# Performance work log

Measured on AMD Instinct MI355X. Metric: run time of the kernel, lower is better.

Reference implementation:

```python
import jax, jax.numpy as jnp
import numpy as np

N = 30000      # nodes
E = 480000     # edges (avg degree 16)
IN = 128       # atom in_channels
ED = 16        # edge_dim
D = 128        # hidden_channels
OUT = 64       # out_channels
L = 4          # num_layers + 1 GCNEConv layers


def setup_inputs() -> dict:
    key = jax.random.key(0)
    ks = jax.random.split(key, 8)
    w = lambda k, sh: (jax.random.normal(k, sh, dtype=jnp.float32) * 0.05)
    return {
        "x": jax.random.normal(ks[0], (N, IN), dtype=jnp.float32),
        "edge_index": jax.random.randint(ks[1], (2, E), 0, N, dtype=jnp.int64),
        "edge_attr": jax.random.normal(ks[2], (E, ED), dtype=jnp.float32),
        "W_atom": w(ks[3], (IN, D)), "b_atom": jnp.zeros((D,), jnp.float32),
        "W_bond": w(ks[4], (ED, D)), "b_bond": jnp.zeros((D,), jnp.float32),
        "W_seq": w(ks[5], (L, D, D)), "b_seq": jnp.zeros((L, D), jnp.float32),
        "W_lin": w(ks[6], (2 * D, OUT)), "b_lin": jnp.zeros((OUT,), jnp.float32),
    }


def _aggregate(h_bond, idx_i, n):
    # CMPNN 'message_booster': elementwise sum_agg * max_agg over incoming edges
    sum_agg = jax.ops.segment_sum(h_bond, idx_i, num_segments=n)
    max_agg = jax.ops.segment_max(h_bond, idx_i, num_segments=n)
    max_agg = jnp.where(jnp.isfinite(max_agg), max_agg, 0.0)  # empty segments -> 0
    return sum_agg * max_agg


def reference(x, edge_index, edge_attr, W_atom, b_atom, W_bond, b_bond,
              W_seq, b_seq, W_lin, b_lin):
    n = x.shape[0]
    idx_i = edge_index[0]  # flow='target_to_source' -> i is edge_index[0]
    idx_j = edge_index[1]

    x_proj = jax.nn.relu(x @ W_atom + b_atom)          # [N, D]
    h_atom = x_proj
    h_bond = jax.nn.relu(edge_attr @ W_bond + b_bond)  # [E, D]

    # first L-1 convs: node update + edge update
    for l in range(L - 1):
        msg = _aggregate(h_bond, idx_i, n)             # [N, D]
        h_atom = h_atom * msg                          # inner_product communicator
        # edge_update: x[edge_index_i] - edge_attr[edge_index_j] (node-index gather
        # into edge tensor, faithful to the original code; valid since E > N)
        bond = h_atom[idx_i] - h_bond[idx_j]           # [E, D]
        h_bond = jax.nn.relu(bond @ W_seq[l] + b_seq[l])

    # last conv: only the node output is used downstream
    msg = _aggregate(h_bond, idx_i, n)
    aggr_atom_message = h_atom * msg

    # top-level communicator (inner_product): hidden_state * message
    h_atom = h_atom * aggr_atom_message
    out = jnp.concatenate([h_atom, x_proj], axis=1) @ W_lin + b_lin  # [N, OUT]
    return out
```

## Files before the change

### kernel.cpp

```cpp
#include <hip/hip_runtime.h>
#include <hip/hip_bf16.h>

#define DD 128
#define SCB 256
#define CE  512
#define CB  512

typedef __attribute__((ext_vector_type(8))) short bf16x8;
typedef __attribute__((ext_vector_type(4))) float f32x4;

__device__ __forceinline__ unsigned bf16_rne(float f) {
    unsigned u = __float_as_uint(f);
    return (u + 0x7fffu + ((u >> 16) & 1u)) >> 16;
}

__global__ __launch_bounds__(256)
void hist_kernel(const int* __restrict__ idx_i, int* __restrict__ cnt, int E)
{
    const int e = blockIdx.x * 256 + threadIdx.x;
    if (e < E) atomicAdd(&cnt[idx_i[e]], 1);
}

__global__ __launch_bounds__(SCB)
void scan1_kernel(const int* __restrict__ cnt, int* __restrict__ exc,
                  int* __restrict__ bsum, int n)
{
    __shared__ int s[SCB];
    const int i = blockIdx.x * SCB + (int)threadIdx.x;
    const int v = (i < n) ? cnt[i] : 0;
    s[threadIdx.x] = v;
    __syncthreads();
    #pragma unroll
    for (int off = 1; off < SCB; off <<= 1) {
        int t = (threadIdx.x >= off) ? s[threadIdx.x - off] : 0;
        __syncthreads();
        s[threadIdx.x] += t;
        __syncthreads();
    }
    if (i < n) exc[i] = s[threadIdx.x] - v;
    if (threadIdx.x == SCB - 1) bsum[blockIdx.x] = s[threadIdx.x];
}

__global__ __launch_bounds__(SCB)
void scan2_kernel(int* __restrict__ bsum, int nb)
{
    __shared__ int s[SCB];
    const int v = (threadIdx.x < nb) ? bsum[threadIdx.x] : 0;
    s[threadIdx.x] = v;
    __syncthreads();
    #pragma unroll
    for (int off = 1; off < SCB; off <<= 1) {
        int t = (threadIdx.x >= off) ? s[threadIdx.x - off] : 0;
        __syncthreads();
        s[threadIdx.x] += t;
        __syncthreads();
    }
    if (threadIdx.x < nb) bsum[threadIdx.x] = s[threadIdx.x] - v;
}

__global__ __launch_bounds__(SCB)
void scan3_kernel(int* __restrict__ exc, const int* __restrict__ bsum, int n)
{
    const int i = blockIdx.x * SCB + (int)threadIdx.x;
    if (i < n) exc[i] += bsum[i >> 8];
}

__global__ __launch_bounds__(256)
void scatter_kernel(const int* __restrict__ idx_i, const int* __restrict__ idx_j,
                    int* __restrict__ cursor, int* __restrict__ perm,
                    int* __restrict__ si, int* __restrict__ sj, int E)
{
    const int e = blockIdx.x * 256 + threadIdx.x;
    if (e < E) {
        const int n = idx_i[e];
        const int p = atomicAdd(&cursor[n], 1);
        perm[p] = e;
        si[p] = n;
        sj[p] = idx_j[e];
    }
}

__global__ __launch_bounds__(1024)
void gemm128_mfma_kernel(float* __restrict__ A0, const float* __restrict__ A1,
                         int nA, int nTotal,
                         const float* __restrict__ W, const float* __restrict__ bias,
                         int bias_limit, int do_relu, int update,
                         float* __restrict__ sum_agg, int* __restrict__ max_agg,
                         float* __restrict__ out0, float* __restrict__ out1,
                         int ntiles)
{
    __shared__ __align__(16) unsigned char SM[131584];
    char*  const Whi = (char*)SM;
    char*  const Wlo = (char*)SM + 32768;
    char*  const Ahi = (char*)SM + 65536;
    char*  const Alo = (char*)SM + 98304;
    float* const Wf  = (float*)(SM + 65536);
    float* const bs  = (float*)(SM + 131072);

    const int t = (int)threadIdx.x;

    {
        const float4* Wg = (const float4*)W;
        float4* Wd = (float4*)Wf;
        #pragma unroll
        for (int i = 0; i < 4; ++i) Wd[t + i * 1024] = Wg[t + i * 1024];
        if (t < DD) bs[t] = bias ? bias[t] : 0.f;
    }
    __syncthreads();
    {
        const int col = t >> 3;
        const int kb  = (t & 7) * 16;
        unsigned h16[16], l16[16];
        #pragma unroll
        for (int j = 0; j < 16; ++j) {
            const float w = Wf[(size_t)(kb + j) * DD + col];
            const unsigned hb = bf16_rne(w);
            const float hf = __uint_as_float(hb << 16);
            h16[j] = hb;
            l16[j] = bf16_rne(w - hf);
        }
        #pragma unroll
        for (int c = 0; c < 2; ++c) {
            uint4 ph, pl;
            ph.x = h16[c*8+0] | (h16[c*8+1] << 16);
            ph.y = h16[c*8+2] | (h16[c*8+3] << 16);
            ph.z = h16[c*8+4] | (h16[c*8+5] << 16);
            ph.w = h16[c*8+6] | (h16[c*8+7] << 16);
            pl.x = l16[c*8+0] | (l16[c*8+1] << 16);
            pl.y = l16[c*8+2] | (l16[c*8+3] << 16);
            pl.z = l16[c*8+4] | (l16[c*8+5] << 16);
            pl.w = l16[c*8+6] | (l16[c*8+7] << 16);
            const int off = ((col * 256 + (kb + c * 8) * 2)) ^ ((col & 7) << 4);
            *(uint4*)(Whi + off) = ph;
            *(uint4*)(Wlo + off) = pl;
        }
    }

    const int w  = t >> 6;
    const int l  = t & 63;
    const int wm = w >> 2;
    const int wn = w & 3;
    const int g  = l >> 4;
    const int q  = l & 15;

    for (int tile = blockIdx.x; tile < ntiles; tile += gridDim.x) {
        const int e0 = tile * 128;
        __syncthreads();

        #pragma unroll
        for (int i = 0; i < 2; ++i) {
            const int task = t + i * 1024;
            const int row  = task >> 4;
            const int c    = task & 15;
            const int rr = min(e0 + row, nTotal - 1);
            float d[8];
            if (rr < nA) {
                float* ph0 = A0 + (size_t)rr * DD + c * 8;
                const float4 a0 = *(const float4*)ph0;
                const float4 a1 = *(const float4*)(ph0 + 4);
                if (update) {
                    float* sp = sum_agg + (size_t)rr * DD + c * 8;
                    int*   mp = max_agg + (size_t)rr * DD + c * 8;
                    const float4 s0 = *(const float4*)sp;
                    const float4 s1 = *(const float4*)(sp + 4);
                    const int4   m0 = *(const int4*)mp;
                    const int4   m1 = *(const int4*)(mp + 4);
                    d[0] = a0.x * s0.x * __int_as_float(m0.x);
                    d[1] = a0.y * s0.y * __int_as_float(m0.y);
                    d[2] = a0.z * s0.z * __int_as_float(m0.z);
                    d[3] = a0.w * s0.w * __int_as_float(m0.w);
                    d[4] = a1.x * s1.x * __int_as_float(m1.x);
                    d[5] = a1.y * s1.y * __int_as_float(m1.y);
                    d[6] = a1.z * s1.z * __int_as_float(m1.z);
                    d[7] = a1.w * s1.w * __int_as_float(m1.w);
                    *(float4*)ph0       = make_float4(d[0], d[1], d[2], d[3]);
                    *(float4*)(ph0 + 4) = make_float4(d[4], d[5], d[6], d[7]);
                    *(float4*)sp       = make_float4(0.f, 0.f, 0.f, 0.f);
                    *(float4*)(sp + 4) = make_float4(0.f, 0.f, 0.f, 0.f);
                    *(int4*)mp       = make_int4(0, 0, 0, 0);
                    *(int4*)(mp + 4) = make_int4(0, 0, 0, 0);
                } else {
                    d[0] = a0.x; d[1] = a0.y; d[2] = a0.z; d[3] = a0.w;
                    d[4] = a1.x; d[5] = a1.y; d[6] = a1.z; d[7] = a1.w;
                }
            } else {
                const float* pa = A1 + (size_t)(rr - nA) * DD + c * 8;
                const float4 a0 = *(const float4*)pa;
                const float4 a1 = *(const float4*)(pa + 4);
                d[0] = a0.x; d[1] = a0.y; d[2] = a0.z; d[3] = a0.w;
                d[4] = a1.x; d[5] = a1.y; d[6] = a1.z; d[7] = a1.w;
            }
            unsigned h8[8], l8[8];
            #pragma unroll
            for (int j = 0; j < 8; ++j) {
                const unsigned hb = bf16_rne(d[j]);
                const float hf = __uint_as_float(hb << 16);
                h8[j] = hb;
                l8[j] = bf16_rne(d[j] - hf);
            }
            uint4 ph, pl;
            ph.x = h8[0] | (h8[1] << 16);
            ph.y = h8[2] | (h8[3] << 16);
            ph.z = h8[4] | (h8[5] << 16);
            ph.w = h8[6] | (h8[7] << 16);
            pl.x = l8[0] | (l8[1] << 16);
            pl.y = l8[2] | (l8[3] << 16);
            pl.z = l8[4] | (l8[5] << 16);
            pl.w = l8[6] | (l8[7] << 16);
            const int off = ((row * 256 + c * 16)) ^ ((row & 7) << 4);
            *(uint4*)(Ahi + off) = ph;
            *(uint4*)(Alo + off) = pl;
        }
        __syncthreads();

        f32x4 acc[2][2];
        const f32x4 zero = {0.f, 0.f, 0.f, 0.f};
        acc[0][0] = zero; acc[0][1] = zero; acc[1][0] = zero; acc[1][1] = zero;

        #pragma unroll
        for (int ks = 0; ks < 4; ++ks) {
            const int kbyte = ks * 64 + g * 16;
            bf16x8 ah[2], al[2], bh[2], bl[2];
            #pragma unroll
            for (int m = 0; m < 2; ++m) {
                const int row = wm * 32 + m * 16 + q;
                const int off = (row * 256 + kbyte) ^ ((row & 7) << 4);
                ah[m] = *(const bf16x8*)(Ahi + off);
                al[m] = *(const bf16x8*)(Alo + off);
            }
            #pragma unroll
            for (int n = 0; n < 2; ++n) {
                const int colv = wn * 32 + n * 16 + q;
                const int off = (colv * 256 + kbyte) ^ ((colv & 7) << 4);
                bh[n] = *(const bf16x8*)(Whi + off);
                bl[n] = *(const bf16x8*)(Wlo + off);
            }
            #pragma unroll
            for (int m = 0; m < 2; ++m)
                #pragma unroll
                for (int n = 0; n < 2; ++n)
                    acc[m][n] = __builtin_amdgcn_mfma_f32_16x16x32_bf16(ah[m], bh[n], acc[m][n], 0, 0, 0);
            #pragma unroll
            for (int m = 0; m < 2; ++m)
                #pragma unroll
                for (int n = 0; n < 2; ++n)
                    acc[m][n] = __builtin_amdgcn_mfma_f32_16x16x32_bf16(ah[m], bl[n], acc[m][n], 0, 0, 0);
            #pragma unroll
            for (int m = 0; m < 2; ++m)
                #pragma unroll
                for (int n = 0; n < 2; ++n)
                    acc[m][n] = __builtin_amdgcn_mfma_f32_16x16x32_bf16(al[m], bh[n], acc[m][n], 0, 0, 0);
        }

        #pragma unroll
        for (int n = 0; n < 2; ++n) {
            const int colv = wn * 32 + n * 16 + q;
            const float bv = bs[colv];
            #pragma unroll
            for (int m = 0; m < 2; ++m) {
                #pragma unroll
                for (int r = 0; r < 4; ++r) {
                    const int row = e0 + wm * 32 + m * 16 + g * 4 + r;
                    if (row < nTotal) {
                        float v = acc[m][n][r] + ((row < bias_limit) ? bv : 0.f);
                        if (do_relu) v = fmaxf(v, 0.f);
                        out0[(size_t)row * DD + colv] = v;
                        if (out1) out1[(size_t)row * DD + colv] = v;
                    }
                }
            }
        }
    }
}

__global__ __launch_bounds__(512)
void bond_pass_kernel(const float* __restrict__ edge_attr,
                      const float* __restrict__ Wb, const float* __restrict__ bb,
                      const int* __restrict__ si, const int* __restrict__ perm,
                      float* __restrict__ h_head0,
                      float* __restrict__ sum_agg, int* __restrict__ max_agg,
                      int E, int N)
{
    __shared__ __align__(16) float ea_s[CB][16];
    __shared__ int si_s[CB], pm_s[CB];

    const int p0b = blockIdx.x * CB;
    if (p0b >= E) return;
    const int t = (int)threadIdx.x;

    for (int i = t; i < CB; i += 512) {
        const int p = min(p0b + i, E - 1);
        si_s[i] = si[p];
        pm_s[i] = perm[p];
    }
    for (int task = t; task < CB * 4; task += 512) {
        const int row = task >> 2;
        const int c4  = task & 3;
        const int p = min(p0b + row, E - 1);
        const int orig = perm[p];
        *(float4*)(&ea_s[row][c4 * 4]) =
            *(const float4*)(edge_attr + (size_t)orig * 16 + c4 * 4);
    }
    __syncthreads();

    const int w    = t >> 6;
    const int lane = t & 63;
    const int c    = lane * 2;
    const int q0   = w * 64;
    const int pg0  = p0b + q0;
    if (pg0 >= E) return;

    float wc0[16], wc1[16];
    #pragma unroll
    for (int k = 0; k < 16; ++k) {
        const float2 wv = *(const float2*)(Wb + k * DD + c);
        wc0[k] = wv.x; wc1[k] = wv.y;
    }
    const float2 bc = *(const float2*)(bb + c);

    const int firstNode = si_s[q0];
    const int lastNode  = si_s[q0 + 63];

    int curNode = firstNode;
    float2 rs = make_float2(0.f, 0.f), rm = make_float2(0.f, 0.f);

    #define BP_FLUSH()                                                           \
    {                                                                            \
        if (curNode == firstNode || curNode == lastNode) {                       \
            atomicAdd(&sum_agg[(size_t)curNode * DD + c],     rs.x);             \
            atomicAdd(&sum_agg[(size_t)curNode * DD + c + 1], rs.y);             \
            atomicMax(&max_agg[(size_t)curNode * DD + c],     __float_as_int(rm.x)); \
            atomicMax(&max_agg[(size_t)curNode * DD + c + 1], __float_as_int(rm.y)); \
        } else {                                                                 \
            *(float2*)(sum_agg + (size_t)curNode * DD + c) = rs;                 \
            *(int2*)(max_agg + (size_t)curNode * DD + c) =                       \
                make_int2(__float_as_int(rm.x), __float_as_int(rm.y));           \
        }                                                                        \
    }

    #pragma unroll 4
    for (int kk = 0; kk < 64; ++kk) {
        const int i = si_s[q0 + kk];
        if (i != curNode) {
            BP_FLUSH();
            curNode = i;
            rs = make_float2(0.f, 0.f);
            rm = make_float2(0.f, 0.f);
        }
        const float4* ear = (const float4*)(&ea_s[q0 + kk][0]);
        const float4 e0 = ear[0], e1 = ear[1], e2 = ear[2], e3 = ear[3];
        float ax = bc.x, ay = bc.y;
        ax = fmaf(e0.x, wc0[ 0], ax);  ay = fmaf(e0.x, wc1[ 0], ay);
        ax = fmaf(e0.y, wc0[ 1], ax);  ay = fmaf(e0.y, wc1[ 1], ay);
        ax = fmaf(e0.z, wc0[ 2], ax);  ay = fmaf(e0.z, wc1[ 2], ay);
        ax = fmaf(e0.w, wc0[ 3], ax);  ay = fmaf(e0.w, wc1[ 3], ay);
        ax = fmaf(e1.x, wc0[ 4], ax);  ay = fmaf(e1.x, wc1[ 4], ay);
        ax = fmaf(e1.y, wc0[ 5], ax);  ay = fmaf(e1.y, wc1[ 5], ay);
        ax = fmaf(e1.z, wc0[ 6], ax);  ay = fmaf(e1.z, wc1[ 6], ay);
        ax = fmaf(e1.w, wc0[ 7], ax);  ay = fmaf(e1.w, wc1[ 7], ay);
        ax = fmaf(e2.x, wc0[ 8], ax);  ay = fmaf(e2.x, wc1[ 8], ay);
        ax = fmaf(e2.y, wc0[ 9], ax);  ay = fmaf(e2.y, wc1[ 9], ay);
        ax = fmaf(e2.z, wc0[10], ax);  ay = fmaf(e2.z, wc1[10], ay);
        ax = fmaf(e2.w, wc0[11], ax);  ay = fmaf(e2.w, wc1[11], ay);
        ax = fmaf(e3.x, wc0[12], ax);  ay = fmaf(e3.x, wc1[12], ay);
        ax = fmaf(e3.y, wc0[13], ax);  ay = fmaf(e3.y, wc1[13], ay);
        ax = fmaf(e3.z, wc0[14], ax);  ay = fmaf(e3.z, wc1[14], ay);
        ax = fmaf(e3.w, wc0[15], ax);  ay = fmaf(e3.w, wc1[15], ay);
        float2 v;
        v.x = fmaxf(ax, 0.f);
        v.y = fmaxf(ay, 0.f);
        if (pg0 + kk >= E) { v.x = 0.f; v.y = 0.f; }
        rs.x += v.x; rs.y += v.y;
        rm.x = fmaxf(rm.x, v.x); rm.y = fmaxf(rm.y, v.y);
        if (pg0 + kk < E) {
            const int orig = pm_s[q0 + kk];
            if (orig < N) *(float2*)(h_head0 + (size_t)orig * DD + c) = v;
        }
    }
    BP_FLUSH();
    #undef BP_FLUSH
}

__global__ __launch_bounds__(512)
void edge_pass_kernel(const float* __restrict__ PQ,
                      const int* __restrict__ si, const int* __restrict__ sj,
                      const int* __restrict__ perm,
                      float* __restrict__ head_next, int store_head,
                      float* __restrict__ sum_agg, int* __restrict__ max_agg,
                      int E, int N)
{
    __shared__ int si_s[CE], sj_s[CE], pm_s[CE];
    const int p0b = blockIdx.x * CE;
    if (p0b >= E) return;
    const int t = (int)threadIdx.x;
    for (int i = t; i < CE; i += 512) {
        const int p = min(p0b + i, E - 1);
        si_s[i] = si[p];
        sj_s[i] = sj[p];
        pm_s[i] = perm[p];
    }
    __syncthreads();

    const int w    = t >> 6;
    const int lane = t & 63;
    const int c    = lane * 2;
    const int q0   = w * 64;
    const int pg0  = p0b + q0;
    if (pg0 >= E) return;

    const int firstNode = si_s[q0];
    const int lastNode  = si_s[q0 + 63];

    const float* __restrict__ Qbase = PQ + (size_t)N * DD + c;

    float2 qa = *(const float2*)(Qbase + (size_t)sj_s[q0 + 0] * DD);
    float2 qb = *(const float2*)(Qbase + (size_t)sj_s[q0 + 1] * DD);
    float2 qc = *(const float2*)(Qbase + (size_t)sj_s[q0 + 2] * DD);
    float2 qd = *(const float2*)(Qbase + (size_t)sj_s[q0 + 3] * DD);
    float2 qe = *(const float2*)(Qbase + (size_t)sj_s[q0 + 4] * DD);
    float2 qf = *(const float2*)(Qbase + (size_t)sj_s[q0 + 5] * DD);
    float2 qg = *(const float2*)(Qbase + (size_t)sj_s[q0 + 6] * DD);
    float2 qh = *(const float2*)(Qbase + (size_t)sj_s[q0 + 7] * DD);

    int curNode = firstNode;
    float2 Pi = *(const float2*)(PQ + (size_t)curNode * DD + c);
    float2 rs = make_float2(0.f, 0.f), rm = make_float2(0.f, 0.f);

    #define EP_FLUSH()                                                           \
    {                                                                            \
        if (curNode == firstNode || curNode == lastNode) {                       \
            atomicAdd(&sum_agg[(size_t)curNode * DD + c],     rs.x);             \
            atomicAdd(&sum_agg[(size_t)curNode * DD + c + 1], rs.y);             \
            atomicMax(&max_agg[(size_t)curNode * DD + c],     __float_as_int(rm.x)); \
            atomicMax(&max_agg[(size_t)curNode * DD + c + 1], __float_as_int(rm.y)); \
        } else {                                                                 \
            *(float2*)(sum_agg + (size_t)curNode * DD + c) = rs;                 \
            *(int2*)(max_agg + (size_t)curNode * DD + c) =                       \
                make_int2(__float_as_int(rm.x), __float_as_int(rm.y));           \
        }                                                                        \
    }

    #define EP_STEP(K, QREG)                                                     \
    {                                                                            \
        const int kk = (K);                                                      \
        const int i = si_s[q0 + kk];                                             \
        if (i != curNode) {                                                      \
            EP_FLUSH();                                                          \
            curNode = i;                                                         \
            Pi = *(const float2*)(PQ + (size_t)i * DD + c);                      \
            rs = make_float2(0.f, 0.f);                                          \
            rm = make_float2(0.f, 0.f);                                          \
        }                                                                        \
        float2 v;                                                                \
        v.x = fmaxf(Pi.x - QREG.x, 0.f);                                         \
        v.y = fmaxf(Pi.y - QREG.y, 0.f);                                         \
        if (pg0 + kk >= E) { v.x = 0.f; v.y = 0.f; }                             \
        rs.x += v.x; rs.y += v.y;                                                \
        rm.x = fmaxf(rm.x, v.x); rm.y = fmaxf(rm.y, v.y);                        \
        if (store_head && (pg0 + kk) < E) {                                      \
            const int orig = pm_s[q0 + kk];                                      \
            if (orig < N) *(float2*)(head_next + (size_t)orig * DD + c) = v;     \
        }                                                                        \
        if (kk + 8 < 64)                                                         \
            QREG = *(const float2*)(Qbase + (size_t)sj_s[q0 + kk + 8] * DD);     \
    }

    #pragma unroll
    for (int k = 0; k < 64; k += 8) {
        EP_STEP(k + 0, qa);
        EP_STEP(k + 1, qb);
        EP_STEP(k + 2, qc);
        EP_STEP(k + 3, qd);
        EP_STEP(k + 4, qe);
        EP_STEP(k + 5, qf);
        EP_STEP(k + 6, qg);
        EP_STEP(k + 7, qh);
    }
    EP_FLUSH();
    #undef EP_STEP
    #undef EP_FLUSH
}

__global__ __launch_bounds__(512, 2)
void final_mfma_kernel(const float* __restrict__ h, const float* __restrict__ sum_agg,
                       const int* __restrict__ max_agg, const float* __restrict__ xp,
                       const float* __restrict__ Wl, const float* __restrict__ bl,
                       float* __restrict__ out, int N)
{
    __shared__ __align__(16) unsigned char SM[65808];
    char*  const Whi = (char*)SM;
    char*  const Wlo = (char*)SM + 32768;
    float* const Wf  = (float*)SM;
    float* const bs  = (float*)(SM + 65536);

    const int t = (int)threadIdx.x;
    {
        const float4* Wg = (const float4*)Wl;
        float4* Wd = (float4*)Wf;
        #pragma unroll
        for (int i = 0; i < 8; ++i) Wd[t + i * 512] = Wg[t + i * 512];
        if (t < 64) bs[t] = bl[t];
    }
    __syncthreads();
    {
        const int col = t & 63;
        const int kb  = (t >> 6) * 32;
        float v[32];
        #pragma unroll
        for (int j = 0; j < 32; ++j) v[j] = Wf[(size_t)(kb + j) * 64 + col];
        __syncthreads();
        #pragma unroll
        for (int c = 0; c < 4; ++c) {
            unsigned h8[8], l8[8];
            #pragma unroll
            for (int j = 0; j < 8; ++j) {
                const float w0 = v[c * 8 + j];
                const unsigned hb = bf16_rne(w0);
                h8[j] = hb;
                l8[j] = bf16_rne(w0 - __uint_as_float(hb << 16));
            }
            uint4 ph, pl;
            ph.x = h8[0] | (h8[1] << 16); ph.y = h8[2] | (h8[3] << 16);
            ph.z = h8[4] | (h8[5] << 16); ph.w = h8[6] | (h8[7] << 16);
            pl.x = l8[0] | (l8[1] << 16); pl.y = l8[2] | (l8[3] << 16);
            pl.z = l8[4] | (l8[5] << 16); pl.w = l8[6] | (l8[7] << 16);
            const int off = (col * 512 + (kb + c * 8) * 2) ^ ((col & 7) << 4);
            *(uint4*)(Whi + off) = ph;
            *(uint4*)(Wlo + off) = pl;
        }
    }
    __syncthreads();

    const int w  = t >> 6;
    const int l  = t & 63;
    const int wm = w >> 1;
    const int wn = w & 1;
    const int g  = l >> 4;
    const int q  = l & 15;
    const int r0 = (int)blockIdx.x * 128;

    f32x4 acc[2][2];
    const f32x4 zero = {0.f, 0.f, 0.f, 0.f};
    acc[0][0] = zero; acc[0][1] = zero; acc[1][0] = zero; acc[1][1] = zero;

    #pragma unroll
    for (int ks = 0; ks < 8; ++ks) {
        const int kf = (ks & 3) * 32 + g * 8;
        bf16x8 ah[2], al[2];
        #pragma unroll
        for (int m = 0; m < 2; ++m) {
            const int rr = min(r0 + wm * 32 + m * 16 + q, N - 1);
            float d[8];
            if (ks < 4) {
                const float* ph = h       + (size_t)rr * DD + kf;
                const float* ps = sum_agg + (size_t)rr * DD + kf;
                const int*   pm = max_agg + (size_t)rr * DD + kf;
                const float4 a0 = *(const float4*)ph;
                const float4 a1 = *(const float4*)(ph + 4);
                const float4 s0 = *(const float4*)ps;
                const float4 s1 = *(const float4*)(ps + 4);
                const int4   i0 = *(const int4*)pm;
                const int4   i1 = *(const int4*)(pm + 4);
                d[0] = a0.x * a0.x * s0.x * __int_as_float(i0.x);
                d[1] = a0.y * a0.y * s0.y * __int_as_float(i0.y);
                d[2] = a0.z * a0.z * s0.z * __int_as_float(i0.z);
                d[3] = a0.w * a0.w * s0.w * __int_as_float(i0.w);
                d[4] = a1.x * a1.x * s1.x * __int_as_float(i1.x);
                d[5] = a1.y * a1.y * s1.y * __int_as_float(i1.y);
                d[6] = a1.z * a1.z * s1.z * __int_as_float(i1.z);
                d[7] = a1.w * a1.w * s1.w * __int_as_float(i1.w);
            } else {
                const float* pa = xp + (size_t)rr * DD + kf;
                const float4 a0 = *(const float4*)pa;
                const float4 a1 = *(const float4*)(pa + 4);
                d[0] = a0.x; d[1] = a0.y; d[2] = a0.z; d[3] = a0.w;
                d[4] = a1.x; d[5] = a1.y; d[6] = a1.z; d[7] = a1.w;
            }
            unsigned h8[8], l8[8];
            #pragma unroll
            for (int j = 0; j < 8; ++j) {
                const unsigned hb = bf16_rne(d[j]);
                h8[j] = hb;
                l8[j] = bf16_rne(d[j] - __uint_as_float(hb << 16));
            }
            uint4 ph2, pl2;
            ph2.x = h8[0] | (h8[1] << 16); ph2.y = h8[2] | (h8[3] << 16);
            ph2.z = h8[4] | (h8[5] << 16); ph2.w = h8[6] | (h8[7] << 16);
            pl2.x = l8[0] | (l8[1] << 16); pl2.y = l8[2] | (l8[3] << 16);
            pl2.z = l8[4] | (l8[5] << 16); pl2.w = l8[6] | (l8[7] << 16);
            ah[m] = *(bf16x8*)&ph2;
            al[m] = *(bf16x8*)&pl2;
        }
        bf16x8 bh[2], blo[2];
        #pragma unroll
        for (int n = 0; n < 2; ++n) {
            const int colv = wn * 32 + n * 16 + q;
            const int off = (colv * 512 + ks * 64 + g * 16) ^ ((colv & 7) << 4);
            bh[n]  = *(const bf16x8*)(Whi + off);
            blo[n] = *(const bf16x8*)(Wlo + off);
        }
        #pragma unroll
        for (int m = 0; m < 2; ++m)
            #pragma unroll
            for (int n = 0; n < 2; ++n) {
                acc[m][n] = __builtin_amdgcn_mfma_f32_16x16x32_bf16(ah[m], bh[n],  acc[m][n], 0, 0, 0);
                acc[m][n] = __builtin_amdgcn_mfma_f32_16x16x32_bf16(ah[m], blo[n], acc[m][n], 0, 0, 0);
                acc[m][n] = __builtin_amdgcn_mfma_f32_16x16x32_bf16(al[m], bh[n],  acc[m][n], 0, 0, 0);
            }
    }

    #pragma unroll
    for (int n = 0; n < 2; ++n) {
        const int colv = wn * 32 + n * 16 + q;
        const float bv = bs[colv];
        #pragma unroll
        for (int m = 0; m < 2; ++m) {
            #pragma unroll
            for (int r = 0; r < 4; ++r) {
                const int row = r0 + wm * 32 + m * 16 + g * 4 + r;
                if (row < N) out[(size_t)row * 64 + colv] = acc[m][n][r] + bv;
            }
        }
    }
}

extern "C" void kernel_launch(void* const* d_in, const int* in_sizes, int n_in,
                              void* d_out, int out_size, void* d_ws, size_t ws_size,
                              hipStream_t stream)
{
    const float* x         = (const float*)d_in[0];
    const int*   edge_idx  = (const int*)d_in[1];
    const float* edge_attr = (const float*)d_in[2];
    const float* W_atom    = (const float*)d_in[3];
    const float* b_atom    = (const float*)d_in[4];
    const float* W_bond    = (const float*)d_in[5];
    const float* b_bond    = (const float*)d_in[6];
    const float* W_seq     = (const float*)d_in[7];
    const float* b_seq     = (const float*)d_in[8];
    const float* W_lin     = (const float*)d_in[9];
    const float* b_lin     = (const float*)d_in[10];
    float* out = (float*)d_out;

    const int N = in_sizes[0] / DD;
    const int E = in_sizes[1] / 2;
    const int* idx_i = edge_idx;
    const int* idx_j = edge_idx + E;

    const size_t nd = (size_t)N * DD;
    float* ws      = (float*)d_ws;
    float* x_proj  = ws;
    float* h_atom  = x_proj + nd;
    float* head    = h_atom + nd;
    float* sum_agg = head + nd;
    int*   max_agg = (int*)(sum_agg + nd);
    float* PQ      = (float*)(max_agg + nd);
    int*   cnt     = (int*)(PQ + 2 * nd);
    int*   cursor  = cnt + N;
    int*   bsum    = cursor + N;
    int*   perm    = bsum + 256;
    int*   si      = perm + E;
    int*   sj      = si + E;

    hipMemsetAsync(cnt, 0, (size_t)N * 4, stream);
    hist_kernel<<<(E + 255) / 256, 256, 0, stream>>>(idx_i, cnt, E);
    const int nb_scan = (N + SCB - 1) / SCB;
    scan1_kernel<<<nb_scan, SCB, 0, stream>>>(cnt, cursor, bsum, N);
    scan2_kernel<<<1, SCB, 0, stream>>>(bsum, nb_scan);
    scan3_kernel<<<nb_scan, SCB, 0, stream>>>(cursor, bsum, N);
    scatter_kernel<<<(E + 255) / 256, 256, 0, stream>>>(idx_i, idx_j, cursor, perm, si, sj, E);

    hipMemsetAsync(sum_agg, 0, nd * 4, stream);
    hipMemsetAsync(max_agg, 0, nd * 4, stream);

    const int ntiles_n = (N + 127) / 128;
    gemm128_mfma_kernel<<<min(ntiles_n, 256), 1024, 0, stream>>>(
        (float*)x, x, N, N, W_atom, b_atom, N, 1, 0, nullptr, nullptr,
        x_proj, h_atom, ntiles_n);

    bond_pass_kernel<<<(E + CB - 1) / CB, 512, 0, stream>>>(
        edge_attr, W_bond, b_bond, si, perm, head, sum_agg, max_agg, E, N);

    const int ntiles_pq = (2 * N + 127) / 128;
    const int ep_blocks = (E + CE - 1) / CE;
    for (int l = 0; l < 3; ++l) {
        gemm128_mfma_kernel<<<256, 1024, 0, stream>>>(
            h_atom, head, N, 2 * N, W_seq + (size_t)l * DD * DD,
            b_seq + (size_t)l * DD, N, 0, 1, sum_agg, max_agg,
            PQ, nullptr, ntiles_pq);
        edge_pass_kernel<<<ep_blocks, 512, 0, stream>>>(
            PQ, si, sj, perm, head, (l < 2) ? 1 : 0, sum_agg, max_agg, E, N);
    }

    final_mfma_kernel<<<(N + 127) / 128, 512, 0, stream>>>(
        h_atom, sum_agg, (const int*)max_agg, x_proj, W_lin, b_lin, out, N);
}
```

Measured before the change: 395.3 us.

## Keep split-bf16 weights in registers and shrink GEMM blocks to 512 threads

The 128x128 GEMM kernel no longer stages the fp32 weight matrix and its hi/lo bf16 split in LDS. Each wave now owns a 16-column slice and keeps its hi/lo weight fragments in registers, while shared memory holds only the A tile (64KB instead of about 128KB). Blocks drop to 512 threads with one tile each, launching a full grid instead of a persistent 256-block grid. This removes the shared-memory weight reads and raises possible occupancy. The cost is that every block re-reads and re-splits W from global memory, and each wave now holds 8 accumulators plus weight registers, which raises register pressure.

```diff
diff --git a/kernel.cpp b/kernel.cpp
--- a/kernel.cpp
+++ b/kernel.cpp
@@ -80,7 +80,7 @@
     }
 }
 
-__global__ __launch_bounds__(1024)
+__global__ __launch_bounds__(512, 4)
 void gemm128_mfma_kernel(float* __restrict__ A0, const float* __restrict__ A1,
                          int nA, int nTotal,
                          const float* __restrict__ W, const float* __restrict__ bias,
@@ -89,67 +89,45 @@
                          float* __restrict__ out0, float* __restrict__ out1,
                          int ntiles)
 {
-    __shared__ __align__(16) unsigned char SM[131584];
-    char*  const Whi = (char*)SM;
-    char*  const Wlo = (char*)SM + 32768;
-    char*  const Ahi = (char*)SM + 65536;
-    char*  const Alo = (char*)SM + 98304;
-    float* const Wf  = (float*)(SM + 65536);
-    float* const bs  = (float*)(SM + 131072);
+    __shared__ __align__(16) unsigned char SM[65536];
+    char* const Ahi = (char*)SM;
+    char* const Alo = (char*)SM + 32768;
 
     const int t = (int)threadIdx.x;
-
-    {
-        const float4* Wg = (const float4*)W;
-        float4* Wd = (float4*)Wf;
-        #pragma unroll
-        for (int i = 0; i < 4; ++i) Wd[t + i * 1024] = Wg[t + i * 1024];
-        if (t < DD) bs[t] = bias ? bias[t] : 0.f;
-    }
-    __syncthreads();
-    {
-        const int col = t >> 3;
-        const int kb  = (t & 7) * 16;
-        unsigned h16[16], l16[16];
-        #pragma unroll
-        for (int j = 0; j < 16; ++j) {
-            const float w = Wf[(size_t)(kb + j) * DD + col];
-            const unsigned hb = bf16_rne(w);
-            const float hf = __uint_as_float(hb << 16);
-            h16[j] = hb;
-            l16[j] = bf16_rne(w - hf);
-        }
-        #pragma unroll
-        for (int c = 0; c < 2; ++c) {
-            uint4 ph, pl;
-            ph.x = h16[c*8+0] | (h16[c*8+1] << 16);
-            ph.y = h16[c*8+2] | (h16[c*8+3] << 16);
-            ph.z = h16[c*8+4] | (h16[c*8+5] << 16);
-            ph.w = h16[c*8+6] | (h16[c*8+7] << 16);
-            pl.x = l16[c*8+0] | (l16[c*8+1] << 16);
-            pl.y = l16[c*8+2] | (l16[c*8+3] << 16);
-            pl.z = l16[c*8+4] | (l16[c*8+5] << 16);
-            pl.w = l16[c*8+6] | (l16[c*8+7] << 16);
-            const int off = ((col * 256 + (kb + c * 8) * 2)) ^ ((col & 7) << 4);
-            *(uint4*)(Whi + off) = ph;
-            *(uint4*)(Wlo + off) = pl;
-        }
-    }
-
-    const int w  = t >> 6;
-    const int l  = t & 63;
-    const int wm = w >> 2;
-    const int wn = w & 3;
-    const int g  = l >> 4;
-    const int q  = l & 15;
+    const int w = t >> 6;
+    const int l = t & 63;
+    const int g = l >> 4;
+    const int q = l & 15;
+    const int colv = w * 16 + q;
+
+    bf16x8 wh[4], wl[4];
+    #pragma unroll
+    for (int ks = 0; ks < 4; ++ks) {
+        unsigned h8[8], l8[8];
+        #pragma unroll
+        for (int j = 0; j < 8; ++j) {
+            const float w0 = W[(size_t)(ks * 32 + g * 8 + j) * DD + colv];
+            const unsigned hb = bf16_rne(w0);
+            h8[j] = hb;
+            l8[j] = bf16_rne(w0 - __uint_as_float(hb << 16));
+        }
+        uint4 ph, pl;
+        ph.x = h8[0] | (h8[1] << 16); ph.y = h8[2] | (h8[3] << 16);
+        ph.z = h8[4] | (h8[5] << 16); ph.w = h8[6] | (h8[7] << 16);
+        pl.x = l8[0] | (l8[1] << 16); pl.y = l8[2] | (l8[3] << 16);
+        pl.z = l8[4] | (l8[5] << 16); pl.w = l8[6] | (l8[7] << 16);
+        wh[ks] = *(bf16x8*)&ph;
+        wl[ks] = *(bf16x8*)&pl;
+    }
+    const float bv = bias ? bias[colv] : 0.f;
 
     for (int tile = blockIdx.x; tile < ntiles; tile += gridDim.x) {
         const int e0 = tile * 128;
         __syncthreads();
 
         #pragma unroll
-        for (int i = 0; i < 2; ++i) {
-            const int task = t + i * 1024;
+        for (int i = 0; i < 4; ++i) {
+            const int task = t + i * 512;
             const int row  = task >> 4;
             const int c    = task & 15;
             const int rr = min(e0 + row, nTotal - 1);
@@ -194,79 +172,50 @@
             #pragma unroll
             for (int j = 0; j < 8; ++j) {
                 const unsigned hb = bf16_rne(d[j]);
-                const float hf = __uint_as_float(hb << 16);
                 h8[j] = hb;
-                l8[j] = bf16_rne(d[j] - hf);
+                l8[j] = bf16_rne(d[j] - __uint_as_float(hb << 16));
             }
             uint4 ph, pl;
-            ph.x = h8[0] | (h8[1] << 16);
-            ph.y = h8[2] | (h8[3] << 16);
-            ph.z = h8[4] | (h8[5] << 16);
-            ph.w = h8[6] | (h8[7] << 16);
-            pl.x = l8[0] | (l8[1] << 16);
-            pl.y = l8[2] | (l8[3] << 16);
-            pl.z = l8[4] | (l8[5] << 16);
-            pl.w = l8[6] | (l8[7] << 16);
+            ph.x = h8[0] | (h8[1] << 16); ph.y = h8[2] | (h8[3] << 16);
+            ph.z = h8[4] | (h8[5] << 16); ph.w = h8[6] | (h8[7] << 16);
+            pl.x = l8[0] | (l8[1] << 16); pl.y = l8[2] | (l8[3] << 16);
+            pl.z = l8[4] | (l8[5] << 16); pl.w = l8[6] | (l8[7] << 16);
             const int off = ((row * 256 + c * 16)) ^ ((row & 7) << 4);
             *(uint4*)(Ahi + off) = ph;
             *(uint4*)(Alo + off) = pl;
         }
         __syncthreads();
 
-        f32x4 acc[2][2];
+        f32x4 acc[8];
         const f32x4 zero = {0.f, 0.f, 0.f, 0.f};
-        acc[0][0] = zero; acc[0][1] = zero; acc[1][0] = zero; acc[1][1] = zero;
+        #pragma unroll
+        for (int m = 0; m < 8; ++m) acc[m] = zero;
 
         #pragma unroll
         for (int ks = 0; ks < 4; ++ks) {
             const int kbyte = ks * 64 + g * 16;
-            bf16x8 ah[2], al[2], bh[2], bl[2];
             #pragma unroll
-            for (int m = 0; m < 2; ++m) {
-                const int row = wm * 32 + m * 16 + q;
+            for (int m = 0; m < 8; ++m) {
+                const int row = m * 16 + q;
                 const int off = (row * 256 + kbyte) ^ ((row & 7) << 4);
-                ah[m] = *(const bf16x8*)(Ahi + off);
-                al[m] = *(const bf16x8*)(Alo + off);
-            }
+                const bf16x8 ah = *(const bf16x8*)(Ahi + off);
+                const bf16x8 al = *(const bf16x8*)(Alo + off);
+                acc[m] = __builtin_amdgcn_mfma_f32_16x16x32_bf16(ah, wh[ks], acc[m], 0, 0, 0);
+                acc[m] = __builtin_amdgcn_mfma_f32_16x16x32_bf16(ah, wl[ks], acc[m], 0, 0, 0);
+                acc[m] = __builtin_amdgcn_mfma_f32_16x16x32_bf16(al, wh[ks], acc[m], 0, 0, 0);
+            }
+        }
+
+        #pragma unroll
+        for (int m = 0; m < 8; ++m) {
             #pragma unroll
-            for (int n = 0; n < 2; ++n) {
-                const int colv = wn * 32 + n * 16 + q;
-                const int off = (colv * 256 + kbyte) ^ ((colv & 7) << 4);
-                bh[n] = *(const bf16x8*)(Whi + off);
-                bl[n] = *(const bf16x8*)(Wlo + off);
-            }
-            #pragma unroll
-            for (int m = 0; m < 2; ++m)
-                #pragma unroll
-                for (int n = 0; n < 2; ++n)
-                    acc[m][n] = __builtin_amdgcn_mfma_f32_16x16x32_bf16(ah[m], bh[n], acc[m][n], 0, 0, 0);
-            #pragma unroll
-            for (int m = 0; m < 2; ++m)
-                #pragma unroll
-                for (int n = 0; n < 2; ++n)
-                    acc[m][n] = __builtin_amdgcn_mfma_f32_16x16x32_bf16(ah[m], bl[n], acc[m][n], 0, 0, 0);
-            #pragma unroll
-            for (int m = 0; m < 2; ++m)
-                #pragma unroll
-                for (int n = 0; n < 2; ++n)
-                    acc[m][n] = __builtin_amdgcn_mfma_f32_16x16x32_bf16(al[m], bh[n], acc[m][n], 0, 0, 0);
-        }
-
-        #pragma unroll
-        for (int n = 0; n < 2; ++n) {
-            const int colv = wn * 32 + n * 16 + q;
-            const float bv = bs[colv];
-            #pragma unroll
-            for (int m = 0; m < 2; ++m) {
-                #pragma unroll
-                for (int r = 0; r < 4; ++r) {
-                    const int row = e0 + wm * 32 + m * 16 + g * 4 + r;
-                    if (row < nTotal) {
-                        float v = acc[m][n][r] + ((row < bias_limit) ? bv : 0.f);
-                        if (do_relu) v = fmaxf(v, 0.f);
-                        out0[(size_t)row * DD + colv] = v;
-                        if (out1) out1[(size_t)row * DD + colv] = v;
-                    }
+            for (int r = 0; r < 4; ++r) {
+                const int row = e0 + m * 16 + g * 4 + r;
+                if (row < nTotal) {
+                    float v = acc[m][r] + ((row < bias_limit) ? bv : 0.f);
+                    if (do_relu) v = fmaxf(v, 0.f);
+                    out0[(size_t)row * DD + colv] = v;
+                    if (out1) out1[(size_t)row * DD + colv] = v;
                 }
             }
         }
@@ -673,7 +622,7 @@
     hipMemsetAsync(max_agg, 0, nd * 4, stream);
 
     const int ntiles_n = (N + 127) / 128;
-    gemm128_mfma_kernel<<<min(ntiles_n, 256), 1024, 0, stream>>>(
+    gemm128_mfma_kernel<<<ntiles_n, 512, 0, stream>>>(
         (float*)x, x, N, N, W_atom, b_atom, N, 1, 0, nullptr, nullptr,
         x_proj, h_atom, ntiles_n);
 
@@ -683,7 +632,7 @@
     const int ntiles_pq = (2 * N + 127) / 128;
     const int ep_blocks = (E + CE - 1) / CE;
     for (int l = 0; l < 3; ++l) {
-        gemm128_mfma_kernel<<<256, 1024, 0, stream>>>(
+        gemm128_mfma_kernel<<<ntiles_pq, 512, 0, stream>>>(
             h_atom, head, N, 2 * N, W_seq + (size_t)l * DD * DD,
             b_seq + (size_t)l * DD, N, 0, 1, sum_agg, max_agg,
             PQ, nullptr, ntiles_pq);
```

New measurement: 389.4 us. No clear change (-1.5%).
